# Optimization experiments

Hardware: AMD Instinct MI355X
Metric: run time of the kernel (lower is better)

## Reference

```python
import jax, jax.numpy as jnp
import numpy as np

EMBED_DIM = 1024
NUM_HEADS = 16
HEAD_DIM = EMBED_DIM // NUM_HEADS


def setup_inputs() -> dict:
    key = jax.random.key(0)
    ks = jax.random.split(key, 7)
    B, S, E = 8, 1024, EMBED_DIM
    # xavier-uniform-like scale for in_proj_weight [3E, E]
    bound_in = float(np.sqrt(6.0 / (3 * E + E)))
    bound_out = float(np.sqrt(6.0 / (E + E)))
    return {
        "q": jax.random.normal(ks[0], (B, S, E), jnp.float32),
        "k": jax.random.normal(ks[1], (B, S, E), jnp.float32),
        "v": jax.random.normal(ks[2], (B, S, E), jnp.float32),
        "in_proj_weight": jax.random.uniform(ks[3], (3 * E, E), jnp.float32, -bound_in, bound_in),
        "in_proj_bias": jnp.zeros((3 * E,), jnp.float32),
        "out_proj_weight": jax.random.uniform(ks[4], (E, E), jnp.float32, -bound_out, bound_out),
        "out_proj_bias": jnp.zeros((E,), jnp.float32),
    }


def reference(q, k, v, in_proj_weight, in_proj_bias, out_proj_weight, out_proj_bias):
    B, S, E = q.shape
    H, D = NUM_HEADS, HEAD_DIM
    w_q, w_k, w_v = jnp.split(in_proj_weight, 3, axis=0)
    b_q, b_k, b_v = jnp.split(in_proj_bias, 3, axis=0)
    # packed in-projection: linear(x, W, b) = x @ W.T + b
    qp = q @ w_q.T + b_q
    kp = k @ w_k.T + b_k
    vp = v @ w_v.T + b_v
    # [B, S, E] -> [B, H, S, D]
    qh = qp.reshape(B, S, H, D).transpose(0, 2, 1, 3)
    kh = kp.reshape(B, S, H, D).transpose(0, 2, 1, 3)
    vh = vp.reshape(B, S, H, D).transpose(0, 2, 1, 3)
    scale = D ** -0.5
    # explicit full attention in fp32 (matches original fp32 cast path)
    scores = jnp.einsum("bhqd,bhkd->bhqk", qh, kh) * scale
    attn = jax.nn.softmax(scores, axis=-1)
    ctx = jnp.einsum("bhqk,bhkd->bhqd", attn, vh)  # [B, H, S, D]
    ctx = ctx.transpose(0, 2, 1, 3).reshape(B, S, E)
    out = ctx @ out_proj_weight.T + out_proj_bias
    return out
```

## Files before the change

### kernel.cpp

```cpp
#include <hip/hip_runtime.h>
#include <stdint.h>

#define TOK 8192
#define EDIM 1024
#define NH 16
#define HD 64
#define SEQ 1024
#define BATCH 8

typedef short bf16x8 __attribute__((ext_vector_type(8)));
typedef short bf16x4 __attribute__((ext_vector_type(4)));
typedef float f32x4 __attribute__((ext_vector_type(4)));
typedef float f32x16 __attribute__((ext_vector_type(16)));
typedef unsigned int u32x2 __attribute__((ext_vector_type(2)));
typedef unsigned int u32x4 __attribute__((ext_vector_type(4)));

__device__ __forceinline__ short f2bf(float f) {
  union { float f; uint32_t u; } c; c.f = f;
  uint32_t u = c.u;
  u += 0x7FFFu + ((u >> 16) & 1u);
  return (short)(u >> 16);
}
__device__ __forceinline__ float bf2f(short h) {
  union { uint32_t u; float f; } c; c.u = ((uint32_t)(uint16_t)h) << 16;
  return c.f;
}
__device__ __forceinline__ uint32_t bfr(float f) {
  union { float f; uint32_t u; } c; c.f = f;
  return (c.u + 0x8000u) >> 16;
}
__device__ __forceinline__ uint32_t cvtpk(float lo, float hi_) {
  uint32_t r;
  asm("v_cvt_pk_bf16_f32 %0, %1, %2" : "=v"(r) : "v"(lo), "v"(hi_));
  return r;
}

#define GLDS16(ldsp, gp) __builtin_amdgcn_global_load_lds( \
    (__attribute__((address_space(1))) void*)(gp),          \
    (__attribute__((address_space(3))) void*)(ldsp), 16, 0, 0)

__global__ __launch_bounds__(256) void cast_all(
    const float* __restrict__ q, const float* __restrict__ k,
    const float* __restrict__ v, const float* __restrict__ wi,
    const float* __restrict__ wo, short* __restrict__ dst) {
  const size_t NTOK = (size_t)TOK * EDIM;
  const size_t NWI = 3u * EDIM * EDIM;
  size_t i = ((size_t)blockIdx.x * 256 + threadIdx.x) * 4;
  const float* src;
  if (i < NTOK) src = q + i;
  else if (i < 2 * NTOK) src = k + (i - NTOK);
  else if (i < 3 * NTOK) src = v + (i - 2 * NTOK);
  else if (i < 3 * NTOK + NWI) src = wi + (i - 3 * NTOK);
  else src = wo + (i - 3 * NTOK - NWI);
  float4 f = *(const float4*)src;
  bf16x4 o;
  o[0] = f2bf(f.x); o[1] = f2bf(f.y); o[2] = f2bf(f.z); o[3] = f2bf(f.w);
  *(bf16x4*)(dst + i) = o;
}

#define GEMM_TILE9(KT, VMC, DOSTAGE)                                           \
  {                                                                            \
    asm volatile("s_waitcnt vmcnt(" VMC ")" ::: "memory");                     \
    __builtin_amdgcn_s_barrier();                                              \
    const short* Ab = lds + ((KT) & 3) * 12288;                                \
    const short* Bb = Ab + 8192;                                               \
    bf16x8 af[4], bv[4];                                                       \
    _Pragma("unroll")                                                          \
    for (int mi = 0; mi < 4; mi++)                                             \
      af[mi] = *(const bf16x8*)&Ab[(wrBase + mi * 16 + fr) * 32 + fg * 8];     \
    _Pragma("unroll")                                                          \
    for (int ni = 0; ni < 4; ni++)                                             \
      bv[ni] = *(const bf16x8*)&Bb[(wcBase + ni * 16 + fr) * 32 + fg * 8];     \
    if (DOSTAGE) {                                                             \
      char* d_ = (char*)lds + (((KT) + 3) & 3) * 24576 + t * 16;               \
      GLDS16(d_,         aS + ((KT) + 3) * 32);                                \
      GLDS16(d_ + 8192,  aS + ((KT) + 3) * 32 + 128 * 1024);                   \
      GLDS16(d_ + 16384, bS + ((KT) + 3) * 32);                                \
    }                                                                          \
    __builtin_amdgcn_s_setprio(1);                                             \
    _Pragma("unroll")                                                          \
    for (int mi = 0; mi < 4; mi++) {                                           \
      _Pragma("unroll")                                                        \
      for (int ni = 0; ni < 4; ni++)                                           \
        acc[mi][ni] = __builtin_amdgcn_mfma_f32_16x16x32_bf16(                 \
            af[mi], bv[ni], acc[mi][ni], 0, 0, 0);                             \
    }                                                                          \
    __builtin_amdgcn_s_setprio(0);                                             \
  }

template<int MODE>
__global__ __launch_bounds__(512, 1)
void gemm_bt9(const short* __restrict__ Abase, const short* __restrict__ Wbase,
              const float* __restrict__ biasBase, void* __restrict__ outv) {
  __shared__ short lds[49152];

  const int z = (MODE == 0) ? blockIdx.z : 0;
  const size_t NTOK = (size_t)TOK * EDIM;
  const short* A  = Abase + (size_t)z * NTOK;
  const short* Bw = Wbase + (size_t)z * EDIM * EDIM;
  const float* bias = biasBase + z * EDIM;

  const int t = threadIdx.x;
  const int l = t & 63, w = t >> 6;
  const int fr = l & 15, fg = l >> 4;
  const int wrBase = (w >> 1) * 64;
  const int wcBase = (w & 1) * 64;
  const int rowBase = blockIdx.x * 256;
  const int colBase = blockIdx.y * 128;

  f32x4 acc[4][4];
#pragma unroll
  for (int i = 0; i < 4; i++)
#pragma unroll
    for (int j = 0; j < 4; j++) acc[i][j] = (f32x4){0.f, 0.f, 0.f, 0.f};

  const short* aS = A  + (size_t)(rowBase + (t >> 2)) * EDIM + (t & 3) * 8;
  const short* bS = Bw + (size_t)(colBase + (t >> 2)) * EDIM + (t & 3) * 8;

#pragma unroll
  for (int s = 0; s < 3; s++) {
    char* d = (char*)lds + s * 24576 + t * 16;
    GLDS16(d,         aS + s * 32);
    GLDS16(d + 8192,  aS + s * 32 + 128 * 1024);
    GLDS16(d + 16384, bS + s * 32);
  }

#pragma unroll 1
  for (int kt = 0; kt < 30; kt++) {
    GEMM_TILE9(kt, "6", (kt <= 28));
  }
  GEMM_TILE9(30, "3", false);
  GEMM_TILE9(31, "0", false);

#pragma unroll
  for (int mi = 0; mi < 4; mi++)
#pragma unroll
    for (int ni = 0; ni < 4; ni++)
#pragma unroll
      for (int r = 0; r < 4; r++) {
        int grow = rowBase + wrBase + mi * 16 + fg * 4 + r;
        int gcol = colBase + wcBase + ni * 16 + fr;
        float v = acc[mi][ni][r] + bias[gcol];
        if (MODE == 0) {
          int b_ = grow >> 10, s_ = grow & 1023;
          int h_ = gcol >> 6,  d_ = gcol & 63;
          short* outp = (short*)outv + (size_t)z * NTOK;
          size_t idx = (z == 2)
              ? (((size_t)((b_ * NH + h_) * HD + d_) << 10) | s_)
              : (((size_t)((b_ * NH + h_) * SEQ + s_) << 6) | d_);
          outp[idx] = f2bf(v);
        } else {
          ((float*)outv)[(size_t)grow * EDIM + gcol] = v;
        }
      }
}

__global__ __launch_bounds__(512)
void attn_fwd10(const short* __restrict__ proj, short* __restrict__ ctx) {
  __shared__ short lds[16384];

  const int t = threadIdx.x;
  const int l = t & 63, w = t >> 6;
  const int ln = l & 31, hi = l >> 5;

  const int n = blockIdx.x + 4 * (blockIdx.y + 16 * blockIdx.z);
  const int qt = (n >> 3) & 3;
  const int hl = (n & 7) | ((n >> 5) << 3);
  const int h = hl & 15, b = hl >> 4;

  const size_t NTOK = (size_t)TOK * EDIM;
  const size_t headOff = (size_t)(b * NH + h) * SEQ * HD;
  const short* Qp  = proj + headOff;
  const short* Kp  = proj + NTOK + headOff;
  const short* VpT = proj + 2 * NTOK + headOff;

  const int q0 = qt * 256;
  const int qrow = q0 + w * 32 + ln;

  const int sRow = t >> 3;
  const int sColSw = ((t & 7) ^ (sRow & 7)) << 3;
  const short* Ksrc0 = Kp  + (size_t)sRow * HD  + sColSw;
  const short* Vsrc0 = VpT + (size_t)sRow * SEQ + sColSw;

  const float qscale = 0.18033688011112042f;
  bf16x8 bQ[4];
#pragma unroll
  for (int ds = 0; ds < 4; ds++) {
    bf16x8 v = *(const bf16x8*)(Qp + (size_t)qrow * HD + ds * 16 + hi * 8);
#pragma unroll
    for (int j = 0; j < 8; j++) v[j] = (short)bfr(bf2f(v[j]) * qscale);
    bQ[ds] = v;
  }

  float l_acc[4] = {0.f, 0.f, 0.f, 0.f};
  f32x16 ot[2];
#pragma unroll
  for (int i = 0; i < 16; i++) { ot[0][i] = 0.f; ot[1][i] = 0.f; }

  GLDS16((char*)lds + t * 16,        Ksrc0);
  GLDS16((char*)lds + 8192 + t * 16, Vsrc0);
  __syncthreads();

  for (int jt = 0; jt < SEQ / 64; jt++) {
    const int bufByte = (jt & 1) << 14;
    const int nb = bufByte ^ (1 << 14);

    if (jt + 1 < SEQ / 64) {
      GLDS16((char*)lds + nb + t * 16,        Ksrc0 + (size_t)(jt + 1) * 64 * HD);
      GLDS16((char*)lds + nb + 8192 + t * 16, Vsrc0 + (jt + 1) * 64);
    }

    f32x16 sa[2];
#pragma unroll
    for (int i = 0; i < 16; i++) { sa[0][i] = 0.f; sa[1][i] = 0.f; }
    __builtin_amdgcn_s_setprio(1);
#pragma unroll
    for (int ds = 0; ds < 4; ds++) {
#pragma unroll
      for (int kvb = 0; kvb < 2; kvb++) {
        int kv = kvb * 32 + ln;
        bf16x8 aK = *(const bf16x8*)((const char*)lds + bufByte + kv * 128 +
                                     (((ds * 2 + hi) ^ (kv & 7)) << 4));
        sa[kvb] = __builtin_amdgcn_mfma_f32_32x32x16_bf16(aK, bQ[ds], sa[kvb], 0, 0, 0);
      }
    }
    __builtin_amdgcn_s_setprio(0);

#pragma unroll
    for (int i = 0; i < 16; i++) {
      float p0 = exp2f(sa[0][i]);
      float p1 = exp2f(sa[1][i]);
      sa[0][i] = p0; sa[1][i] = p1;
      l_acc[i & 3] += p0 + p1;
    }

    bf16x8 pa[4];
#pragma unroll
    for (int ks = 0; ks < 4; ks++) {
      const int kvb = ks >> 1, hf = (ks & 1) * 8;
      uint32_t A1 = cvtpk(sa[kvb][hf + 0], sa[kvb][hf + 1]);
      uint32_t A2 = cvtpk(sa[kvb][hf + 2], sa[kvb][hf + 3]);
      uint32_t B1 = cvtpk(sa[kvb][hf + 4], sa[kvb][hf + 5]);
      uint32_t B2 = cvtpk(sa[kvb][hf + 6], sa[kvb][hf + 7]);
      u32x4 wds;
#if __has_builtin(__builtin_amdgcn_permlane32_swap)
      u32x2 r13 = __builtin_amdgcn_permlane32_swap(A1, B1, false, false);
      u32x2 r24 = __builtin_amdgcn_permlane32_swap(A2, B2, false, false);
      wds[0] = r13[0]; wds[2] = r13[1];
      wds[1] = r24[0]; wds[3] = r24[1];
#else
      uint32_t send1 = hi ? A1 : B1;
      uint32_t send2 = hi ? A2 : B2;
      uint32_t recv1 = (uint32_t)__shfl_xor((int)send1, 32);
      uint32_t recv2 = (uint32_t)__shfl_xor((int)send2, 32);
      wds[0] = hi ? recv1 : A1;
      wds[1] = hi ? recv2 : A2;
      wds[2] = hi ? B1 : recv1;
      wds[3] = hi ? B2 : recv2;
#endif
      pa[ks] = __builtin_bit_cast(bf16x8, wds);
    }

    const char* VtB = (const char*)lds + bufByte + 8192;
    __builtin_amdgcn_s_setprio(1);
#pragma unroll
    for (int ks = 0; ks < 4; ks++) {
#pragma unroll
      for (int dblk = 0; dblk < 2; dblk++) {
        int d = dblk * 32 + ln;
        bf16x8 aV = *(const bf16x8*)(VtB + d * 128 + (((ks * 2 + hi) ^ (d & 7)) << 4));
        ot[dblk] = __builtin_amdgcn_mfma_f32_32x32x16_bf16(aV, pa[ks], ot[dblk], 0, 0, 0);
      }
    }
    __builtin_amdgcn_s_setprio(0);

    __syncthreads();
  }

  float l_run = (l_acc[0] + l_acc[1]) + (l_acc[2] + l_acc[3]);
  l_run += __shfl_xor(l_run, 32);
  float rl = 1.0f / l_run;

#pragma unroll
  for (int dblk = 0; dblk < 2; dblk++)
#pragma unroll
    for (int r = 0; r < 16; r++) {
      int d = dblk * 32 + (r & 3) + 8 * (r >> 2) + 4 * hi;
      int qrl = w * 32 + ln;
      int byteoff = qrl * 128 + (((d >> 3) ^ (qrl & 7)) << 4) + (d & 7) * 2;
      *(short*)((char*)lds + byteoff) = (short)bfr(ot[dblk][r] * rl);
    }
  __syncthreads();
#pragma unroll
  for (int i = 0; i < 4; i++) {
    int chunk = t * 4 + i;
    int row = chunk >> 3, c8 = chunk & 7;
    bf16x8 vv = *(const bf16x8*)((const char*)lds + row * 128 + ((c8 ^ (row & 7)) << 4));
    *(bf16x8*)(ctx + (size_t)(b * SEQ + q0 + row) * EDIM + h * HD + c8 * 8) = vv;
  }
}

extern "C" void kernel_launch(void* const* d_in, const int* in_sizes, int n_in,
                              void* d_out, int out_size, void* d_ws, size_t ws_size,
                              hipStream_t stream) {
  const float* q  = (const float*)d_in[0];
  const float* k  = (const float*)d_in[1];
  const float* v  = (const float*)d_in[2];
  const float* wi = (const float*)d_in[3];
  const float* bi = (const float*)d_in[4];
  const float* wo = (const float*)d_in[5];
  const float* bo = (const float*)d_in[6];
  float* out = (float*)d_out;

  short* ws = (short*)d_ws;
  const size_t NTOK = (size_t)TOK * EDIM;
  short* qkv_bf   = ws;
  short* w_in_bf  = qkv_bf + 3 * NTOK;
  short* w_out_bf = w_in_bf + 3 * (size_t)EDIM * EDIM;
  short* proj_bf  = w_out_bf + (size_t)EDIM * EDIM;
  short* ctx_bf   = qkv_bf;

  const size_t totalCast = 3 * NTOK + 3 * (size_t)EDIM * EDIM + (size_t)EDIM * EDIM;
  cast_all<<<dim3((unsigned)(totalCast / 4 / 256)), 256, 0, stream>>>(q, k, v, wi, wo, qkv_bf);

  gemm_bt9<0><<<dim3(TOK / 256, EDIM / 128, 3), 512, 0, stream>>>(qkv_bf, w_in_bf, bi, proj_bf);
  attn_fwd10<<<dim3(SEQ / 256, NH, BATCH), 512, 0, stream>>>(proj_bf, ctx_bf);
  gemm_bt9<1><<<dim3(TOK / 256, EDIM / 128, 1), 512, 0, stream>>>(ctx_bf, w_out_bf, bo, out);
}
```

Baseline: 172.3 us.

## Swizzle GEMM LDS tiles and stage transposed V epilogue through LDS

Applies an XOR swizzle to the 16-byte chunk index, both when the global-to-LDS staging writes the GEMM tiles and when MFMA fragments are read, to cut LDS bank conflicts. For the V projection (z==2), the transposed output is first packed into LDS with a swizzled layout. It is then written to global memory as contiguous 16-byte vectors instead of scattered 2-byte strided stores. This adds an extra LDS pass and barrier in the epilogue and relies on cvtpk and on the shared buffer being free after the main loop.

```diff
diff --git a/kernel.cpp b/kernel.cpp
--- a/kernel.cpp
+++ b/kernel.cpp
@@ -67,10 +67,10 @@
     bf16x8 af[4], bv[4];                                                       \
     _Pragma("unroll")                                                          \
     for (int mi = 0; mi < 4; mi++)                                             \
-      af[mi] = *(const bf16x8*)&Ab[(wrBase + mi * 16 + fr) * 32 + fg * 8];     \
+      af[mi] = *(const bf16x8*)&Ab[(wrBase + mi * 16 + fr) * 32 + fgsw * 8];   \
     _Pragma("unroll")                                                          \
     for (int ni = 0; ni < 4; ni++)                                             \
-      bv[ni] = *(const bf16x8*)&Bb[(wcBase + ni * 16 + fr) * 32 + fg * 8];     \
+      bv[ni] = *(const bf16x8*)&Bb[(wcBase + ni * 16 + fr) * 32 + fgsw * 8];   \
     if (DOSTAGE) {                                                             \
       char* d_ = (char*)lds + (((KT) + 3) & 3) * 24576 + t * 16;               \
       GLDS16(d_,         aS + ((KT) + 3) * 32);                                \
@@ -103,6 +103,7 @@
   const int t = threadIdx.x;
   const int l = t & 63, w = t >> 6;
   const int fr = l & 15, fg = l >> 4;
+  const int fgsw = fg ^ ((fr >> 1) & 3);
   const int wrBase = (w >> 1) * 64;
   const int wcBase = (w & 1) * 64;
   const int rowBase = blockIdx.x * 256;
@@ -114,8 +115,9 @@
 #pragma unroll
     for (int j = 0; j < 4; j++) acc[i][j] = (f32x4){0.f, 0.f, 0.f, 0.f};
 
-  const short* aS = A  + (size_t)(rowBase + (t >> 2)) * EDIM + (t & 3) * 8;
-  const short* bS = Bw + (size_t)(colBase + (t >> 2)) * EDIM + (t & 3) * 8;
+  const int sChunk = (t & 3) ^ ((t >> 3) & 3);
+  const short* aS = A  + (size_t)(rowBase + (t >> 2)) * EDIM + sChunk * 8;
+  const short* bS = Bw + (size_t)(colBase + (t >> 2)) * EDIM + sChunk * 8;
 
 #pragma unroll
   for (int s = 0; s < 3; s++) {
@@ -132,27 +134,53 @@
   GEMM_TILE9(30, "3", false);
   GEMM_TILE9(31, "0", false);
 
-#pragma unroll
-  for (int mi = 0; mi < 4; mi++)
-#pragma unroll
-    for (int ni = 0; ni < 4; ni++)
-#pragma unroll
-      for (int r = 0; r < 4; r++) {
-        int grow = rowBase + wrBase + mi * 16 + fg * 4 + r;
-        int gcol = colBase + wcBase + ni * 16 + fr;
-        float v = acc[mi][ni][r] + bias[gcol];
-        if (MODE == 0) {
-          int b_ = grow >> 10, s_ = grow & 1023;
-          int h_ = gcol >> 6,  d_ = gcol & 63;
-          short* outp = (short*)outv + (size_t)z * NTOK;
-          size_t idx = (z == 2)
-              ? (((size_t)((b_ * NH + h_) * HD + d_) << 10) | s_)
-              : (((size_t)((b_ * NH + h_) * SEQ + s_) << 6) | d_);
-          outp[idx] = f2bf(v);
-        } else {
-          ((float*)outv)[(size_t)grow * EDIM + gcol] = v;
+  if (MODE == 0 && z == 2) {
+#pragma unroll
+    for (int mi = 0; mi < 4; mi++)
+#pragma unroll
+      for (int ni = 0; ni < 4; ni++) {
+        int dloc = wcBase + ni * 16 + fr;
+        int sl = wrBase + mi * 16 + fg * 4;
+        float b0 = bias[colBase + dloc];
+        u32x2 pk;
+        pk[0] = cvtpk(acc[mi][ni][0] + b0, acc[mi][ni][1] + b0);
+        pk[1] = cvtpk(acc[mi][ni][2] + b0, acc[mi][ni][3] + b0);
+        int byteoff = dloc * 512 + (((sl >> 3) ^ (dloc & 31)) << 4) + ((fg & 1) << 3);
+        *(u32x2*)((char*)lds + byteoff) = pk;
+      }
+    __syncthreads();
+    short* outp = (short*)outv + 2 * NTOK;
+    const int b_ = rowBase >> 10;
+    const int s0 = rowBase & 1023;
+#pragma unroll
+    for (int i = 0; i < 8; i++) {
+      int id = i * 512 + t;
+      int dloc = id >> 5, c = id & 31;
+      bf16x8 vv = *(const bf16x8*)((char*)lds + dloc * 512 + ((c ^ (dloc & 31)) << 4));
+      int gcol = colBase + dloc;
+      int h_ = gcol >> 6, d_ = gcol & 63;
+      *(bf16x8*)(outp + ((((size_t)((b_ * NH + h_) * HD + d_)) << 10) | (s0 + c * 8))) = vv;
+    }
+  } else {
+#pragma unroll
+    for (int mi = 0; mi < 4; mi++)
+#pragma unroll
+      for (int ni = 0; ni < 4; ni++)
+#pragma unroll
+        for (int r = 0; r < 4; r++) {
+          int grow = rowBase + wrBase + mi * 16 + fg * 4 + r;
+          int gcol = colBase + wcBase + ni * 16 + fr;
+          float v = acc[mi][ni][r] + bias[gcol];
+          if (MODE == 0) {
+            int b_ = grow >> 10, s_ = grow & 1023;
+            int h_ = gcol >> 6,  d_ = gcol & 63;
+            short* outp = (short*)outv + (size_t)z * NTOK;
+            outp[((size_t)((b_ * NH + h_) * SEQ + s_) << 6) | d_] = f2bf(v);
+          } else {
+            ((float*)outv)[(size_t)grow * EDIM + gcol] = v;
+          }
         }
-      }
+  }
 }
 
 __global__ __launch_bounds__(512)
```

After: 156.8 us. -9.0%, faster.
